# Optimization experiments

Hardware: AMD Instinct MI355X
Metric: run time of the kernel (lower is better)

## Reference

```python
import jax, jax.numpy as jnp
import numpy as np

B, C, L = 4, 512, 4096

def setup_inputs() -> dict:
    key = jax.random.key(0)
    k1, k2, k3, k4 = jax.random.split(key, 4)
    proj_query = jax.random.normal(k1, (B, C, L), dtype=jnp.float32)
    proj_key = jax.random.normal(k2, (B, C, L), dtype=jnp.float32)
    proj_val = jax.random.normal(k3, (B, C, L), dtype=jnp.float32)
    # binary padding mask over key positions, broadcast over query axis
    padding_mask = (jax.random.uniform(k4, (B, 1, L)) < 0.9).astype(jnp.float32)
    return {"proj_query": proj_query, "proj_key": proj_key,
            "proj_val": proj_val, "padding_mask": padding_mask}

def reference(proj_query, proj_key, proj_val, padding_mask):
    c = proj_query.shape[1]
    # energy[b,i,j] = sum_c Q[b,c,i] * K[b,c,j]  -> (B, L1, L2)
    energy = jnp.einsum('bci,bcj->bij', proj_query, proj_key)
    attention = energy / jnp.sqrt(jnp.asarray(c, dtype=energy.dtype))
    attention = attention + jnp.log(padding_mask + 1e-6)
    attention = jax.nn.softmax(attention, axis=-1)
    attention = attention * padding_mask
    attention = attention.transpose(0, 2, 1)  # (B, L2, L1)
    out = jnp.einsum('bcj,bji->bci', proj_val, attention)  # (B, C, L1)
    return out, attention
```

## Files before the change

kernel.cpp:

```cpp
#include <hip/hip_runtime.h>

#define B_ 4
#define C_ 512
#define L_ 4096

typedef __attribute__((ext_vector_type(8))) short bf16x8;
typedef __attribute__((ext_vector_type(4))) float f32x4;

static __device__ __forceinline__ unsigned short f2bf_rne(float f) {
  unsigned u = __float_as_uint(f);
  u += 0x7FFFu + ((u >> 16) & 1u);
  return (unsigned short)(u >> 16);
}
static __device__ __forceinline__ unsigned pack_rne(float a, float b) {
  return (unsigned)f2bf_rne(a) | ((unsigned)f2bf_rne(b) << 16);
}
static __device__ __forceinline__ unsigned pack_trunc(float a, float b) {
  return (__float_as_uint(a) >> 16) | (__float_as_uint(b) & 0xFFFF0000u);
}

static __device__ __forceinline__ void g2lds16(const unsigned short* g,
                                               unsigned short* l) {
  __builtin_amdgcn_global_load_lds(
      (const __attribute__((address_space(1))) unsigned int*)g,
      (__attribute__((address_space(3))) unsigned int*)l, 16, 0, 0);
}

__global__ __launch_bounds__(256) void transpose_cast_k(
    const float* __restrict__ Q, const float* __restrict__ K,
    unsigned short* __restrict__ Qt, unsigned short* __restrict__ Kt) {
  int zb = blockIdx.z;
  int b = zb >> 1;
  const float* src = ((zb & 1) ? K : Q) + (size_t)b * C_ * L_;
  unsigned short* dst = ((zb & 1) ? Kt : Qt) + (size_t)b * L_ * C_;
  int i0 = blockIdx.x * 64, c0 = blockIdx.y * 64;
  __shared__ float tile[64][65];
  int t = threadIdx.x;
  int cr = t >> 2, ig = (t & 3) * 16;
  const float* s = src + (size_t)(c0 + cr) * L_ + i0 + ig;
#pragma unroll
  for (int q = 0; q < 4; ++q) {
    float4 v = *(const float4*)(s + 4 * q);
    tile[cr][ig + 4 * q + 0] = v.x;
    tile[cr][ig + 4 * q + 1] = v.y;
    tile[cr][ig + 4 * q + 2] = v.z;
    tile[cr][ig + 4 * q + 3] = v.w;
  }
  __syncthreads();
  int ir = t >> 2, cg = (t & 3) * 16;
  unsigned wds[8];
#pragma unroll
  for (int k = 0; k < 8; ++k)
    wds[k] = pack_rne(tile[cg + 2 * k][ir], tile[cg + 2 * k + 1][ir]);
  unsigned short* d = dst + (size_t)(i0 + ir) * C_ + c0 + cg;
  uint4 o0, o1;
  o0.x = wds[0]; o0.y = wds[1]; o0.z = wds[2]; o0.w = wds[3];
  o1.x = wds[4]; o1.y = wds[5]; o1.z = wds[6]; o1.w = wds[7];
  *(uint4*)d = o0;
  *(uint4*)(d + 8) = o1;
}

__global__ __launch_bounds__(256) void cast_v_k(
    const float* __restrict__ V, const float* __restrict__ mask,
    unsigned short* __restrict__ Vb) {
  size_t idx = ((size_t)blockIdx.x * 256 + threadIdx.x) * 8;
  int b = (int)(idx >> 21);
  int j = (int)(idx & (L_ - 1));
  float4 v0 = *(const float4*)(V + idx);
  float4 v1 = *(const float4*)(V + idx + 4);
  const float* m = mask + (size_t)b * L_ + j;
  float4 m0 = *(const float4*)m;
  float4 m1 = *(const float4*)(m + 4);
  uint4 o;
  o.x = pack_rne(v0.x * m0.x, v0.y * m0.y);
  o.y = pack_rne(v0.z * m0.z, v0.w * m0.w);
  o.z = pack_rne(v1.x * m1.x, v1.y * m1.y);
  o.w = pack_rne(v1.z * m1.z, v1.w * m1.w);
  *(uint4*)(Vb + idx) = o;
}

__device__ __forceinline__ void gemm_mainloop(
    const unsigned short* Ab, const unsigned short* Bb, int lda, int ldb,
    int Kdim, unsigned short* sA, unsigned short* sB, f32x4 acc[4][4]) {
  int t = threadIdx.x;
  int f0 = t * 8;
  int f1 = 2048 + t * 8;
  int r0 = f0 >> 5, q0 = f0 & 31;
  int r1 = f1 >> 5, q1 = f1 & 31;
  const unsigned short* pA0 = Ab + (size_t)r0 * lda + q0;
  const unsigned short* pA1 = Ab + (size_t)r1 * lda + q1;
  const unsigned short* pB0 = Bb + (size_t)r0 * ldb + q0;
  const unsigned short* pB1 = Bb + (size_t)r1 * ldb + q1;
  int lane = t & 63;
  int quad = lane >> 4;
  int l15 = lane & 15;
  int w = t >> 6;
  int wm = (w & 1) * 64;
  int wn = (w >> 1) * 64;
  for (int kk = 0; kk < Kdim; kk += 32) {
    __syncthreads();
    g2lds16(pA0 + kk, sA + f0);
    g2lds16(pA1 + kk, sA + f1);
    g2lds16(pB0 + kk, sB + f0);
    g2lds16(pB1 + kk, sB + f1);
    __syncthreads();
    bf16x8 aF[4], bF[4];
#pragma unroll
    for (int ti = 0; ti < 4; ++ti)
      aF[ti] = *(const bf16x8*)(sA + (wm + ti * 16 + l15) * 32 + quad * 8);
#pragma unroll
    for (int tj = 0; tj < 4; ++tj)
      bF[tj] = *(const bf16x8*)(sB + (wn + tj * 16 + l15) * 32 + quad * 8);
#pragma unroll
    for (int ti = 0; ti < 4; ++ti)
#pragma unroll
      for (int tj = 0; tj < 4; ++tj)
        acc[ti][tj] = __builtin_amdgcn_mfma_f32_16x16x32_bf16(
            aF[ti], bF[tj], acc[ti][tj], 0, 0, 0);
  }
}

__global__ __launch_bounds__(256) void gemm1_k(
    const unsigned short* __restrict__ Qt, const unsigned short* __restrict__ Kt,
    const float* __restrict__ mask, float* __restrict__ attn,
    float* __restrict__ rowsum) {
  int b = blockIdx.z;
  int i0 = blockIdx.y * 128;
  int j0 = blockIdx.x * 128;
  __shared__ unsigned short sA[128 * 32];
  __shared__ unsigned short sB[128 * 32];
  f32x4 acc[4][4] = {};
  gemm_mainloop(Qt + (size_t)b * L_ * C_ + (size_t)i0 * C_,
                Kt + (size_t)b * L_ * C_ + (size_t)j0 * C_, C_, C_, C_, sA, sB,
                acc);
  int t = threadIdx.x;
  int lane = t & 63;
  int quad = lane >> 4;
  int l15 = lane & 15;
  int w = t >> 6;
  int wm = (w & 1) * 64;
  int wn = (w >> 1) * 64;
  const float scale = 0.04419417382415922f;
  float lm[4];
#pragma unroll
  for (int tj = 0; tj < 4; ++tj) {
    int j = j0 + wn + tj * 16 + l15;
    lm[tj] = __logf(mask[(size_t)b * L_ + j] + 1e-6f);
  }
  float* ab = attn + (size_t)b * L_ * L_;
  float rs[16];
#pragma unroll
  for (int q = 0; q < 16; ++q) rs[q] = 0.f;
#pragma unroll
  for (int ti = 0; ti < 4; ++ti) {
    int irow = i0 + wm + ti * 16 + quad * 4;
#pragma unroll
    for (int r = 0; r < 4; ++r) {
      size_t ro = (size_t)(irow + r) * L_;
#pragma unroll
      for (int tj = 0; tj < 4; ++tj) {
        float x = fminf(acc[ti][tj][r] * scale + lm[tj], 60.f);
        float tv = __expf(x);
        rs[ti * 4 + r] += tv;
        ab[ro + j0 + wn + tj * 16 + l15] = tv;
      }
    }
  }
#pragma unroll
  for (int m = 1; m < 16; m <<= 1)
#pragma unroll
    for (int q = 0; q < 16; ++q) rs[q] += __shfl_xor(rs[q], m, 64);
  if (l15 == 0) {
    float* rb = rowsum + (size_t)b * L_ + i0 + wm;
#pragma unroll
    for (int ti = 0; ti < 4; ++ti)
#pragma unroll
      for (int r = 0; r < 4; ++r)
        atomicAdd(&rb[ti * 16 + quad * 4 + r], rs[ti * 4 + r]);
  }
}

__global__ __launch_bounds__(256) void gemm2_k(
    const unsigned short* __restrict__ Vb, const float* __restrict__ tmat,
    const float* __restrict__ rowsum, float* __restrict__ out) {
  int b = blockIdx.z;
  int c0 = blockIdx.y * 128;
  int i0 = blockIdx.x * 128;
  __shared__ unsigned short sA[128 * 32];
  __shared__ unsigned short sB[128 * 32];
  const unsigned short* Ab = Vb + (size_t)b * C_ * L_ + (size_t)c0 * L_;
  const float* Bb = tmat + (size_t)b * L_ * L_ + (size_t)i0 * L_;
  int t = threadIdx.x;
  int f0 = t * 8;
  int f1 = 2048 + t * 8;
  int r0 = f0 >> 5, q0 = f0 & 31;
  int r1 = f1 >> 5, q1 = f1 & 31;
  const unsigned short* pA0 = Ab + (size_t)r0 * L_ + q0;
  const unsigned short* pA1 = Ab + (size_t)r1 * L_ + q1;
  const float* pB0 = Bb + (size_t)r0 * L_ + q0;
  const float* pB1 = Bb + (size_t)r1 * L_ + q1;
  int lane = t & 63;
  int quad = lane >> 4;
  int l15 = lane & 15;
  int w = t >> 6;
  int wm = (w & 1) * 64;
  int wn = (w >> 1) * 64;
  f32x4 acc[4][4] = {};
  for (int kk = 0; kk < L_; kk += 32) {
    __syncthreads();
    g2lds16(pA0 + kk, sA + f0);
    g2lds16(pA1 + kk, sA + f1);
    float4 x0 = *(const float4*)(pB0 + kk);
    float4 x1 = *(const float4*)(pB0 + kk + 4);
    float4 y0 = *(const float4*)(pB1 + kk);
    float4 y1 = *(const float4*)(pB1 + kk + 4);
    uint4 u0, u1;
    u0.x = pack_trunc(x0.x, x0.y); u0.y = pack_trunc(x0.z, x0.w);
    u0.z = pack_trunc(x1.x, x1.y); u0.w = pack_trunc(x1.z, x1.w);
    u1.x = pack_trunc(y0.x, y0.y); u1.y = pack_trunc(y0.z, y0.w);
    u1.z = pack_trunc(y1.x, y1.y); u1.w = pack_trunc(y1.z, y1.w);
    *(uint4*)(sB + f0) = u0;
    *(uint4*)(sB + f1) = u1;
    __syncthreads();
    bf16x8 aF[4], bF[4];
#pragma unroll
    for (int ti = 0; ti < 4; ++ti)
      aF[ti] = *(const bf16x8*)(sA + (wm + ti * 16 + l15) * 32 + quad * 8);
#pragma unroll
    for (int tj = 0; tj < 4; ++tj)
      bF[tj] = *(const bf16x8*)(sB + (wn + tj * 16 + l15) * 32 + quad * 8);
#pragma unroll
    for (int ti = 0; ti < 4; ++ti)
#pragma unroll
      for (int tj = 0; tj < 4; ++tj)
        acc[ti][tj] = __builtin_amdgcn_mfma_f32_16x16x32_bf16(
            aF[ti], bF[tj], acc[ti][tj], 0, 0, 0);
  }
  float invv[4];
#pragma unroll
  for (int tj = 0; tj < 4; ++tj)
    invv[tj] = 1.0f / rowsum[(size_t)b * L_ + i0 + wn + tj * 16 + l15];
  float* ob = out + (size_t)b * C_ * L_;
#pragma unroll
  for (int ti = 0; ti < 4; ++ti) {
    int crow = c0 + wm + ti * 16 + quad * 4;
#pragma unroll
    for (int r = 0; r < 4; ++r) {
      size_t ro = (size_t)(crow + r) * L_;
#pragma unroll
      for (int tj = 0; tj < 4; ++tj)
        ob[ro + i0 + wn + tj * 16 + l15] = acc[ti][tj][r] * invv[tj];
    }
  }
}

__global__ __launch_bounds__(256) void transpose_scale_k(
    float* __restrict__ attn, const float* __restrict__ rowsum,
    const float* __restrict__ mask) {
  int ti = blockIdx.x, tj = blockIdx.y;
  if (ti > tj) return;
  int b = blockIdx.z;
  float* M = attn + (size_t)b * L_ * L_;
  const float* mk = mask + (size_t)b * L_;
  const float* rs = rowsum + (size_t)b * L_;
  __shared__ float t1[64][65];
  __shared__ float t2[64][65];
  int t = threadIdx.x;
  int r = t >> 2, cg = (t & 3) * 16;
  bool diag = (ti == tj);
  {
    const float* xp = M + (size_t)(ti * 64 + r) * L_ + tj * 64 + cg;
    float invx = 1.0f / rs[ti * 64 + r];
    const float* mx = mk + tj * 64 + cg;
#pragma unroll
    for (int q = 0; q < 4; ++q) {
      float4 v = *(const float4*)(xp + 4 * q);
      float4 m = *(const float4*)(mx + 4 * q);
      t1[r][cg + 4 * q + 0] = v.x * m.x * invx;
      t1[r][cg + 4 * q + 1] = v.y * m.y * invx;
      t1[r][cg + 4 * q + 2] = v.z * m.z * invx;
      t1[r][cg + 4 * q + 3] = v.w * m.w * invx;
    }
  }
  if (!diag) {
    const float* yp = M + (size_t)(tj * 64 + r) * L_ + ti * 64 + cg;
    float invy = 1.0f / rs[tj * 64 + r];
    const float* my = mk + ti * 64 + cg;
#pragma unroll
    for (int q = 0; q < 4; ++q) {
      float4 v = *(const float4*)(yp + 4 * q);
      float4 m = *(const float4*)(my + 4 * q);
      t2[r][cg + 4 * q + 0] = v.x * m.x * invy;
      t2[r][cg + 4 * q + 1] = v.y * m.y * invy;
      t2[r][cg + 4 * q + 2] = v.z * m.z * invy;
      t2[r][cg + 4 * q + 3] = v.w * m.w * invy;
    }
  }
  __syncthreads();
  {
    float* dp = M + (size_t)(tj * 64 + r) * L_ + ti * 64 + cg;
#pragma unroll
    for (int q = 0; q < 4; ++q) {
      float4 o;
      o.x = t1[cg + 4 * q + 0][r];
      o.y = t1[cg + 4 * q + 1][r];
      o.z = t1[cg + 4 * q + 2][r];
      o.w = t1[cg + 4 * q + 3][r];
      *(float4*)(dp + 4 * q) = o;
    }
  }
  if (!diag) {
    float* dp = M + (size_t)(ti * 64 + r) * L_ + tj * 64 + cg;
#pragma unroll
    for (int q = 0; q < 4; ++q) {
      float4 o;
      o.x = t2[cg + 4 * q + 0][r];
      o.y = t2[cg + 4 * q + 1][r];
      o.z = t2[cg + 4 * q + 2][r];
      o.w = t2[cg + 4 * q + 3][r];
      *(float4*)(dp + 4 * q) = o;
    }
  }
}

extern "C" void kernel_launch(void* const* d_in, const int* in_sizes, int n_in,
                              void* d_out, int out_size, void* d_ws,
                              size_t ws_size, hipStream_t stream) {
  const float* Q = (const float*)d_in[0];
  const float* K = (const float*)d_in[1];
  const float* V = (const float*)d_in[2];
  const float* mask = (const float*)d_in[3];

  float* out = (float*)d_out;
  float* attn = out + (size_t)B_ * C_ * L_;

  unsigned short* Qt = (unsigned short*)d_ws;
  unsigned short* Kt = Qt + (size_t)B_ * L_ * C_;
  unsigned short* Vb = Kt + (size_t)B_ * L_ * C_;
  float* rowsum = (float*)(Vb + (size_t)B_ * C_ * L_);

  hipMemsetAsync(rowsum, 0, (size_t)B_ * L_ * sizeof(float), stream);

  transpose_cast_k<<<dim3(L_ / 64, C_ / 64, B_ * 2), 256, 0, stream>>>(Q, K, Qt,
                                                                       Kt);
  cast_v_k<<<dim3((B_ * C_ * L_) / 2048), 256, 0, stream>>>(V, mask, Vb);
  gemm1_k<<<dim3(L_ / 128, L_ / 128, B_), 256, 0, stream>>>(Qt, Kt, mask, attn,
                                                            rowsum);
  gemm2_k<<<dim3(L_ / 128, C_ / 128, B_), 256, 0, stream>>>(Vb, attn, rowsum,
                                                            out);
  transpose_scale_k<<<dim3(64, 64, B_), 256, 0, stream>>>(attn, rowsum, mask);
}
```

Baseline: 812.9 us.

## Store unnormalized attention as bf16 in scratch and split-K the PV GEMM

Gemm1 now writes exp-scores as bf16 into the upper halves of the attention output buffer and a workspace slot, in place of fp32 attention. This halves traffic for the intermediate matrix that gemm2 reads. Gemm2 is split into two K halves that accumulate into a zeroed output with atomics, doubling the grid. Per-batch finalize kernels then normalize and transpose the bf16 data into fp32 attention. The gains come with an extra memset, atomic traffic on the output, a dependence on the workspace size, and ordering hazards from aliasing inside the output buffer.

```diff
diff --git a/kernel.cpp b/kernel.cpp
--- a/kernel.cpp
+++ b/kernel.cpp
@@ -17,6 +17,12 @@
 }
 static __device__ __forceinline__ unsigned pack_trunc(float a, float b) {
   return (__float_as_uint(a) >> 16) | (__float_as_uint(b) & 0xFFFF0000u);
+}
+static __device__ __forceinline__ float bflo2f(unsigned w) {
+  return __uint_as_float(w << 16);
+}
+static __device__ __forceinline__ float bfhi2f(unsigned w) {
+  return __uint_as_float(w & 0xFFFF0000u);
 }
 
 static __device__ __forceinline__ void g2lds16(const unsigned short* g,
@@ -117,6 +123,148 @@
       for (int tj = 0; tj < 4; ++tj)
         acc[ti][tj] = __builtin_amdgcn_mfma_f32_16x16x32_bf16(
             aF[ti], bF[tj], acc[ti][tj], 0, 0, 0);
+  }
+}
+
+
+__global__ __launch_bounds__(256) void gemm1_bf_k(
+    const unsigned short* __restrict__ Qt, const unsigned short* __restrict__ Kt,
+    const float* __restrict__ mask, unsigned short* __restrict__ t0,
+    unsigned short* __restrict__ t1, unsigned short* __restrict__ t2,
+    unsigned short* __restrict__ t3, float* __restrict__ rowsum) {
+  int b = blockIdx.z;
+  unsigned short* tbb = (b == 0) ? t0 : (b == 1) ? t1 : (b == 2) ? t2 : t3;
+  int i0 = blockIdx.y * 128;
+  int j0 = blockIdx.x * 128;
+  __shared__ unsigned short sA[128 * 32];
+  __shared__ unsigned short sB[128 * 32];
+  f32x4 acc[4][4] = {};
+  gemm_mainloop(Qt + (size_t)b * L_ * C_ + (size_t)i0 * C_,
+                Kt + (size_t)b * L_ * C_ + (size_t)j0 * C_, C_, C_, C_, sA, sB,
+                acc);
+  int t = threadIdx.x;
+  int lane = t & 63;
+  int quad = lane >> 4;
+  int l15 = lane & 15;
+  int w = t >> 6;
+  int wm = (w & 1) * 64;
+  int wn = (w >> 1) * 64;
+  const float scale = 0.04419417382415922f;
+  float lm[4], mv[4];
+#pragma unroll
+  for (int tj = 0; tj < 4; ++tj) {
+    int j = j0 + wn + tj * 16 + l15;
+    float m = mask[(size_t)b * L_ + j];
+    mv[tj] = m;
+    lm[tj] = __logf(m + 1e-6f);
+  }
+  float rs[16];
+#pragma unroll
+  for (int q = 0; q < 16; ++q) rs[q] = 0.f;
+#pragma unroll
+  for (int ti = 0; ti < 4; ++ti) {
+    int irow = i0 + wm + ti * 16 + quad * 4;
+#pragma unroll
+    for (int r = 0; r < 4; ++r) {
+      size_t ro = (size_t)(irow + r) * L_;
+#pragma unroll
+      for (int tj = 0; tj < 4; ++tj) {
+        float x = fminf(acc[ti][tj][r] * scale + lm[tj], 60.f);
+        float tv = __expf(x);
+        rs[ti * 4 + r] += tv;
+        tbb[ro + j0 + wn + tj * 16 + l15] = f2bf_rne(tv * mv[tj]);
+      }
+    }
+  }
+#pragma unroll
+  for (int m = 1; m < 16; m <<= 1)
+#pragma unroll
+    for (int q = 0; q < 16; ++q) rs[q] += __shfl_xor(rs[q], m, 64);
+  if (l15 == 0) {
+    float* rb = rowsum + (size_t)b * L_ + i0 + wm;
+#pragma unroll
+    for (int ti = 0; ti < 4; ++ti)
+#pragma unroll
+      for (int r = 0; r < 4; ++r)
+        atomicAdd(&rb[ti * 16 + quad * 4 + r], rs[ti * 4 + r]);
+  }
+}
+
+__global__ __launch_bounds__(256) void gemm2_bf_k(
+    const unsigned short* __restrict__ Vb, const unsigned short* __restrict__ t0,
+    const unsigned short* __restrict__ t1, const unsigned short* __restrict__ t2,
+    const unsigned short* __restrict__ t3, const float* __restrict__ rowsum,
+    float* __restrict__ out) {
+  int z = blockIdx.z;
+  int b = z & 3;
+  int ks = z >> 2;
+  const unsigned short* tbb =
+      (b == 0) ? t0 : (b == 1) ? t1 : (b == 2) ? t2 : t3;
+  int c0 = blockIdx.y * 128;
+  int i0 = blockIdx.x * 128;
+  __shared__ unsigned short sA[128 * 32];
+  __shared__ unsigned short sB[128 * 32];
+  f32x4 acc[4][4] = {};
+  gemm_mainloop(Vb + (size_t)b * C_ * L_ + (size_t)c0 * L_ + ks * (L_ / 2),
+                tbb + (size_t)i0 * L_ + ks * (L_ / 2), L_, L_, L_ / 2, sA, sB,
+                acc);
+  int t = threadIdx.x;
+  int lane = t & 63;
+  int quad = lane >> 4;
+  int l15 = lane & 15;
+  int w = t >> 6;
+  int wm = (w & 1) * 64;
+  int wn = (w >> 1) * 64;
+  float invv[4];
+#pragma unroll
+  for (int tj = 0; tj < 4; ++tj)
+    invv[tj] = 1.0f / rowsum[(size_t)b * L_ + i0 + wn + tj * 16 + l15];
+  float* ob = out + (size_t)b * C_ * L_;
+#pragma unroll
+  for (int ti = 0; ti < 4; ++ti) {
+    int crow = c0 + wm + ti * 16 + quad * 4;
+#pragma unroll
+    for (int r = 0; r < 4; ++r) {
+      size_t ro = (size_t)(crow + r) * L_;
+#pragma unroll
+      for (int tj = 0; tj < 4; ++tj)
+        atomicAdd(&ob[ro + i0 + wn + tj * 16 + l15],
+                  acc[ti][tj][r] * invv[tj]);
+    }
+  }
+}
+
+__global__ __launch_bounds__(256) void finalize_k(
+    const unsigned short* __restrict__ src, const float* __restrict__ rs,
+    float* __restrict__ dst) {
+  int jt = blockIdx.x, it = blockIdx.y;
+  __shared__ float tileT[64][65];
+  int t = threadIdx.x;
+  int r = t >> 2, cg = (t & 3) * 16;
+  int i = it * 64 + r;
+  float inv = 1.0f / rs[i];
+  const unsigned short* sp = src + (size_t)i * L_ + jt * 64 + cg;
+  uint4 u0 = *(const uint4*)sp;
+  uint4 u1 = *(const uint4*)(sp + 8);
+  const unsigned* w0 = (const unsigned*)&u0;
+  const unsigned* w1 = (const unsigned*)&u1;
+#pragma unroll
+  for (int k = 0; k < 4; ++k) {
+    tileT[cg + 2 * k + 0][r] = bflo2f(w0[k]) * inv;
+    tileT[cg + 2 * k + 1][r] = bfhi2f(w0[k]) * inv;
+    tileT[cg + 8 + 2 * k + 0][r] = bflo2f(w1[k]) * inv;
+    tileT[cg + 8 + 2 * k + 1][r] = bfhi2f(w1[k]) * inv;
+  }
+  __syncthreads();
+  float* dp = dst + (size_t)(jt * 64 + r) * L_ + it * 64 + cg;
+#pragma unroll
+  for (int q = 0; q < 4; ++q) {
+    float4 o;
+    o.x = tileT[r][cg + 4 * q + 0];
+    o.y = tileT[r][cg + 4 * q + 1];
+    o.z = tileT[r][cg + 4 * q + 2];
+    o.w = tileT[r][cg + 4 * q + 3];
+    *(float4*)(dp + 4 * q) = o;
   }
 }
 
@@ -334,19 +482,43 @@
   float* out = (float*)d_out;
   float* attn = out + (size_t)B_ * C_ * L_;
 
+  const size_t NQ = (size_t)B_ * L_ * C_;
   unsigned short* Qt = (unsigned short*)d_ws;
-  unsigned short* Kt = Qt + (size_t)B_ * L_ * C_;
-  unsigned short* Vb = Kt + (size_t)B_ * L_ * C_;
-  float* rowsum = (float*)(Vb + (size_t)B_ * C_ * L_);
+  unsigned short* Kt = Qt + NQ;
+  unsigned short* Vb = Kt + NQ;
+  float* rowsum = (float*)(Vb + NQ);
+  unsigned short* tb3 = (unsigned short*)(rowsum + (size_t)B_ * L_);
+
+  const size_t need = NQ * 2 * 3 + (size_t)B_ * L_ * 4 + (size_t)L_ * L_ * 2;
 
   hipMemsetAsync(rowsum, 0, (size_t)B_ * L_ * sizeof(float), stream);
-
   transpose_cast_k<<<dim3(L_ / 64, C_ / 64, B_ * 2), 256, 0, stream>>>(Q, K, Qt,
                                                                        Kt);
   cast_v_k<<<dim3((B_ * C_ * L_) / 2048), 256, 0, stream>>>(V, mask, Vb);
-  gemm1_k<<<dim3(L_ / 128, L_ / 128, B_), 256, 0, stream>>>(Qt, Kt, mask, attn,
-                                                            rowsum);
-  gemm2_k<<<dim3(L_ / 128, C_ / 128, B_), 256, 0, stream>>>(Vb, attn, rowsum,
-                                                            out);
-  transpose_scale_k<<<dim3(64, 64, B_), 256, 0, stream>>>(attn, rowsum, mask);
-}
+
+  if (ws_size >= need) {
+    const size_t SLOT = (size_t)L_ * L_;
+    unsigned short* tb0 = (unsigned short*)(attn + 2 * SLOT);
+    unsigned short* tb1 = (unsigned short*)(attn + 3 * SLOT);
+    unsigned short* tb2 = (unsigned short*)(attn + 3 * SLOT + SLOT / 2);
+    hipMemsetAsync(out, 0, (size_t)B_ * C_ * L_ * sizeof(float), stream);
+    gemm1_bf_k<<<dim3(L_ / 128, L_ / 128, B_), 256, 0, stream>>>(
+        Qt, Kt, mask, tb0, tb1, tb2, tb3, rowsum);
+    gemm2_bf_k<<<dim3(L_ / 128, C_ / 128, B_ * 2), 256, 0, stream>>>(
+        Vb, tb0, tb1, tb2, tb3, rowsum, out);
+    finalize_k<<<dim3(64, 64), 256, 0, stream>>>(tb0, rowsum, attn);
+    finalize_k<<<dim3(64, 64), 256, 0, stream>>>(tb1, rowsum + L_,
+                                                 attn + 1 * SLOT);
+    finalize_k<<<dim3(64, 64), 256, 0, stream>>>(tb2, rowsum + 2 * L_,
+                                                 attn + 2 * SLOT);
+    finalize_k<<<dim3(64, 64), 256, 0, stream>>>(tb3, rowsum + 3 * L_,
+                                                 attn + 3 * SLOT);
+  } else {
+    gemm1_k<<<dim3(L_ / 128, L_ / 128, B_), 256, 0, stream>>>(Qt, Kt, mask,
+                                                              attn, rowsum);
+    gemm2_k<<<dim3(L_ / 128, C_ / 128, B_), 256, 0, stream>>>(Vb, attn, rowsum,
+                                                              out);
+    transpose_scale_k<<<dim3(64, 64, B_), 256, 0, stream>>>(attn, rowsum,
+                                                            mask);
+  }
+}
```

Measured after the change: 719.8 us. -11.5%, faster.

## Store unnormalized masked attention as bf16 and split-K gemm2 with tiled transpose finalize

Applied to the files above, without the earlier changes.

GEMM1 now writes the masked exponentials as bf16 into a workspace instead of fp32 into the output, which halves that intermediate's traffic. GEMM2 reads the bf16 tiles directly through global_load_lds instead of loading fp32 and packing in registers, and splits K in two across the grid with a combine pass. The shared mainloop now stages 64-wide K chunks per barrier pair, and a new finalize kernel normalizes and transposes the bf16 into the fp32 attention output over the full grid. A fallback path aliases buffers into the output and uses atomics when the workspace is too small; rounding the probabilities to bf16 before the fp32 attention output adds rounding error.

```diff
diff --git a/kernel.cpp b/kernel.cpp
--- a/kernel.cpp
+++ b/kernel.cpp
@@ -15,8 +15,11 @@
 static __device__ __forceinline__ unsigned pack_rne(float a, float b) {
   return (unsigned)f2bf_rne(a) | ((unsigned)f2bf_rne(b) << 16);
 }
-static __device__ __forceinline__ unsigned pack_trunc(float a, float b) {
-  return (__float_as_uint(a) >> 16) | (__float_as_uint(b) & 0xFFFF0000u);
+static __device__ __forceinline__ float bflo2f(unsigned w) {
+  return __uint_as_float(w << 16);
+}
+static __device__ __forceinline__ float bfhi2f(unsigned w) {
+  return __uint_as_float(w & 0xFFFF0000u);
 }
 
 static __device__ __forceinline__ void g2lds16(const unsigned short* g,
@@ -79,60 +82,72 @@
   *(uint4*)(Vb + idx) = o;
 }
 
-__device__ __forceinline__ void gemm_mainloop(
+__device__ __forceinline__ void gemm_mainloop64(
     const unsigned short* Ab, const unsigned short* Bb, int lda, int ldb,
     int Kdim, unsigned short* sA, unsigned short* sB, f32x4 acc[4][4]) {
   int t = threadIdx.x;
-  int f0 = t * 8;
-  int f1 = 2048 + t * 8;
-  int r0 = f0 >> 5, q0 = f0 & 31;
-  int r1 = f1 >> 5, q1 = f1 & 31;
-  const unsigned short* pA0 = Ab + (size_t)r0 * lda + q0;
-  const unsigned short* pA1 = Ab + (size_t)r1 * lda + q1;
-  const unsigned short* pB0 = Bb + (size_t)r0 * ldb + q0;
-  const unsigned short* pB1 = Bb + (size_t)r1 * ldb + q1;
+  const unsigned short* pA[4];
+  const unsigned short* pB[4];
+#pragma unroll
+  for (int c = 0; c < 4; ++c) {
+    int e = t * 8 + c * 2048;
+    int kc = e >> 12;
+    int rem = e & 4095;
+    int row = rem >> 5;
+    int col = rem & 31;
+    int off = kc * 32 + col;
+    pA[c] = Ab + (size_t)row * lda + off;
+    pB[c] = Bb + (size_t)row * ldb + off;
+  }
   int lane = t & 63;
   int quad = lane >> 4;
   int l15 = lane & 15;
   int w = t >> 6;
   int wm = (w & 1) * 64;
   int wn = (w >> 1) * 64;
-  for (int kk = 0; kk < Kdim; kk += 32) {
+  for (int kk = 0; kk < Kdim; kk += 64) {
     __syncthreads();
-    g2lds16(pA0 + kk, sA + f0);
-    g2lds16(pA1 + kk, sA + f1);
-    g2lds16(pB0 + kk, sB + f0);
-    g2lds16(pB1 + kk, sB + f1);
+#pragma unroll
+    for (int c = 0; c < 4; ++c) g2lds16(pA[c] + kk, sA + t * 8 + c * 2048);
+#pragma unroll
+    for (int c = 0; c < 4; ++c) g2lds16(pB[c] + kk, sB + t * 8 + c * 2048);
     __syncthreads();
-    bf16x8 aF[4], bF[4];
-#pragma unroll
-    for (int ti = 0; ti < 4; ++ti)
-      aF[ti] = *(const bf16x8*)(sA + (wm + ti * 16 + l15) * 32 + quad * 8);
-#pragma unroll
-    for (int tj = 0; tj < 4; ++tj)
-      bF[tj] = *(const bf16x8*)(sB + (wn + tj * 16 + l15) * 32 + quad * 8);
-#pragma unroll
-    for (int ti = 0; ti < 4; ++ti)
+#pragma unroll
+    for (int kc = 0; kc < 2; ++kc) {
+      bf16x8 aF[4], bF[4];
+#pragma unroll
+      for (int ti = 0; ti < 4; ++ti)
+        aF[ti] = *(const bf16x8*)(sA + kc * 4096 +
+                                  (wm + ti * 16 + l15) * 32 + quad * 8);
 #pragma unroll
       for (int tj = 0; tj < 4; ++tj)
-        acc[ti][tj] = __builtin_amdgcn_mfma_f32_16x16x32_bf16(
-            aF[ti], bF[tj], acc[ti][tj], 0, 0, 0);
-  }
-}
-
-__global__ __launch_bounds__(256) void gemm1_k(
+        bF[tj] = *(const bf16x8*)(sB + kc * 4096 +
+                                  (wn + tj * 16 + l15) * 32 + quad * 8);
+#pragma unroll
+      for (int ti = 0; ti < 4; ++ti)
+#pragma unroll
+        for (int tj = 0; tj < 4; ++tj)
+          acc[ti][tj] = __builtin_amdgcn_mfma_f32_16x16x32_bf16(
+              aF[ti], bF[tj], acc[ti][tj], 0, 0, 0);
+    }
+  }
+}
+
+__global__ __launch_bounds__(256) void gemm1_bf_k(
     const unsigned short* __restrict__ Qt, const unsigned short* __restrict__ Kt,
-    const float* __restrict__ mask, float* __restrict__ attn,
-    float* __restrict__ rowsum) {
+    const float* __restrict__ mask, unsigned short* __restrict__ t0,
+    unsigned short* __restrict__ t1, unsigned short* __restrict__ t2,
+    unsigned short* __restrict__ t3, float* __restrict__ rowsum) {
   int b = blockIdx.z;
+  unsigned short* tbb = (b == 0) ? t0 : (b == 1) ? t1 : (b == 2) ? t2 : t3;
   int i0 = blockIdx.y * 128;
   int j0 = blockIdx.x * 128;
-  __shared__ unsigned short sA[128 * 32];
-  __shared__ unsigned short sB[128 * 32];
+  __shared__ unsigned short sA[8192];
+  __shared__ unsigned short sB[8192];
   f32x4 acc[4][4] = {};
-  gemm_mainloop(Qt + (size_t)b * L_ * C_ + (size_t)i0 * C_,
-                Kt + (size_t)b * L_ * C_ + (size_t)j0 * C_, C_, C_, C_, sA, sB,
-                acc);
+  gemm_mainloop64(Qt + (size_t)b * L_ * C_ + (size_t)i0 * C_,
+                  Kt + (size_t)b * L_ * C_ + (size_t)j0 * C_, C_, C_, C_, sA,
+                  sB, acc);
   int t = threadIdx.x;
   int lane = t & 63;
   int quad = lane >> 4;
@@ -141,13 +156,14 @@
   int wm = (w & 1) * 64;
   int wn = (w >> 1) * 64;
   const float scale = 0.04419417382415922f;
-  float lm[4];
+  float lm[4], mv[4];
 #pragma unroll
   for (int tj = 0; tj < 4; ++tj) {
     int j = j0 + wn + tj * 16 + l15;
-    lm[tj] = __logf(mask[(size_t)b * L_ + j] + 1e-6f);
-  }
-  float* ab = attn + (size_t)b * L_ * L_;
+    float m = mask[(size_t)b * L_ + j];
+    mv[tj] = m;
+    lm[tj] = __logf(m + 1e-6f);
+  }
   float rs[16];
 #pragma unroll
   for (int q = 0; q < 16; ++q) rs[q] = 0.f;
@@ -162,7 +178,7 @@
         float x = fminf(acc[ti][tj][r] * scale + lm[tj], 60.f);
         float tv = __expf(x);
         rs[ti * 4 + r] += tv;
-        ab[ro + j0 + wn + tj * 16 + l15] = tv;
+        tbb[ro + j0 + wn + tj * 16 + l15] = f2bf_rne(tv * mv[tj]);
       }
     }
   }
@@ -180,67 +196,37 @@
   }
 }
 
-__global__ __launch_bounds__(256) void gemm2_k(
-    const unsigned short* __restrict__ Vb, const float* __restrict__ tmat,
-    const float* __restrict__ rowsum, float* __restrict__ out) {
-  int b = blockIdx.z;
+template <bool ATOMIC>
+__global__ __launch_bounds__(256) void gemm2_bf_k(
+    const unsigned short* __restrict__ Vb, const unsigned short* __restrict__ t0,
+    const unsigned short* __restrict__ t1, const unsigned short* __restrict__ t2,
+    const unsigned short* __restrict__ t3, const float* __restrict__ rowsum,
+    float* __restrict__ out, float* __restrict__ out2) {
+  int z = blockIdx.z;
+  int b = z & 3;
+  int ks = z >> 2;
+  const unsigned short* tbb =
+      (b == 0) ? t0 : (b == 1) ? t1 : (b == 2) ? t2 : t3;
   int c0 = blockIdx.y * 128;
   int i0 = blockIdx.x * 128;
-  __shared__ unsigned short sA[128 * 32];
-  __shared__ unsigned short sB[128 * 32];
-  const unsigned short* Ab = Vb + (size_t)b * C_ * L_ + (size_t)c0 * L_;
-  const float* Bb = tmat + (size_t)b * L_ * L_ + (size_t)i0 * L_;
-  int t = threadIdx.x;
-  int f0 = t * 8;
-  int f1 = 2048 + t * 8;
-  int r0 = f0 >> 5, q0 = f0 & 31;
-  int r1 = f1 >> 5, q1 = f1 & 31;
-  const unsigned short* pA0 = Ab + (size_t)r0 * L_ + q0;
-  const unsigned short* pA1 = Ab + (size_t)r1 * L_ + q1;
-  const float* pB0 = Bb + (size_t)r0 * L_ + q0;
-  const float* pB1 = Bb + (size_t)r1 * L_ + q1;
+  __shared__ unsigned short sA[8192];
+  __shared__ unsigned short sB[8192];
+  f32x4 acc[4][4] = {};
+  gemm_mainloop64(Vb + (size_t)b * C_ * L_ + (size_t)c0 * L_ + ks * (L_ / 2),
+                  tbb + (size_t)i0 * L_ + ks * (L_ / 2), L_, L_, L_ / 2, sA, sB,
+                  acc);
+  int t = threadIdx.x;
   int lane = t & 63;
   int quad = lane >> 4;
   int l15 = lane & 15;
   int w = t >> 6;
   int wm = (w & 1) * 64;
   int wn = (w >> 1) * 64;
-  f32x4 acc[4][4] = {};
-  for (int kk = 0; kk < L_; kk += 32) {
-    __syncthreads();
-    g2lds16(pA0 + kk, sA + f0);
-    g2lds16(pA1 + kk, sA + f1);
-    float4 x0 = *(const float4*)(pB0 + kk);
-    float4 x1 = *(const float4*)(pB0 + kk + 4);
-    float4 y0 = *(const float4*)(pB1 + kk);
-    float4 y1 = *(const float4*)(pB1 + kk + 4);
-    uint4 u0, u1;
-    u0.x = pack_trunc(x0.x, x0.y); u0.y = pack_trunc(x0.z, x0.w);
-    u0.z = pack_trunc(x1.x, x1.y); u0.w = pack_trunc(x1.z, x1.w);
-    u1.x = pack_trunc(y0.x, y0.y); u1.y = pack_trunc(y0.z, y0.w);
-    u1.z = pack_trunc(y1.x, y1.y); u1.w = pack_trunc(y1.z, y1.w);
-    *(uint4*)(sB + f0) = u0;
-    *(uint4*)(sB + f1) = u1;
-    __syncthreads();
-    bf16x8 aF[4], bF[4];
-#pragma unroll
-    for (int ti = 0; ti < 4; ++ti)
-      aF[ti] = *(const bf16x8*)(sA + (wm + ti * 16 + l15) * 32 + quad * 8);
-#pragma unroll
-    for (int tj = 0; tj < 4; ++tj)
-      bF[tj] = *(const bf16x8*)(sB + (wn + tj * 16 + l15) * 32 + quad * 8);
-#pragma unroll
-    for (int ti = 0; ti < 4; ++ti)
-#pragma unroll
-      for (int tj = 0; tj < 4; ++tj)
-        acc[ti][tj] = __builtin_amdgcn_mfma_f32_16x16x32_bf16(
-            aF[ti], bF[tj], acc[ti][tj], 0, 0, 0);
-  }
   float invv[4];
 #pragma unroll
   for (int tj = 0; tj < 4; ++tj)
     invv[tj] = 1.0f / rowsum[(size_t)b * L_ + i0 + wn + tj * 16 + l15];
-  float* ob = out + (size_t)b * C_ * L_;
+  float* ob = (ATOMIC ? out : (ks ? out2 : out)) + (size_t)b * C_ * L_;
 #pragma unroll
   for (int ti = 0; ti < 4; ++ti) {
     int crow = c0 + wm + ti * 16 + quad * 4;
@@ -248,78 +234,65 @@
     for (int r = 0; r < 4; ++r) {
       size_t ro = (size_t)(crow + r) * L_;
 #pragma unroll
-      for (int tj = 0; tj < 4; ++tj)
-        ob[ro + i0 + wn + tj * 16 + l15] = acc[ti][tj][r] * invv[tj];
+      for (int tj = 0; tj < 4; ++tj) {
+        float v = acc[ti][tj][r] * invv[tj];
+        if (ATOMIC)
+          atomicAdd(&ob[ro + i0 + wn + tj * 16 + l15], v);
+        else
+          ob[ro + i0 + wn + tj * 16 + l15] = v;
+      }
     }
   }
 }
 
-__global__ __launch_bounds__(256) void transpose_scale_k(
-    float* __restrict__ attn, const float* __restrict__ rowsum,
-    const float* __restrict__ mask) {
-  int ti = blockIdx.x, tj = blockIdx.y;
-  if (ti > tj) return;
+__global__ __launch_bounds__(256) void combine_out_k(
+    float* __restrict__ out, const float* __restrict__ out2) {
+  size_t idx = ((size_t)blockIdx.x * 256 + threadIdx.x) * 8;
+  float4 a0 = *(const float4*)(out + idx);
+  float4 a1 = *(const float4*)(out + idx + 4);
+  float4 b0 = *(const float4*)(out2 + idx);
+  float4 b1 = *(const float4*)(out2 + idx + 4);
+  a0.x += b0.x; a0.y += b0.y; a0.z += b0.z; a0.w += b0.w;
+  a1.x += b1.x; a1.y += b1.y; a1.z += b1.z; a1.w += b1.w;
+  *(float4*)(out + idx) = a0;
+  *(float4*)(out + idx + 4) = a1;
+}
+
+__global__ __launch_bounds__(256) void finalize_all_k(
+    const unsigned short* __restrict__ tb, const float* __restrict__ rowsum,
+    float* __restrict__ attn) {
   int b = blockIdx.z;
-  float* M = attn + (size_t)b * L_ * L_;
-  const float* mk = mask + (size_t)b * L_;
+  const unsigned short* src = tb + (size_t)b * L_ * L_;
   const float* rs = rowsum + (size_t)b * L_;
-  __shared__ float t1[64][65];
-  __shared__ float t2[64][65];
+  float* dst = attn + (size_t)b * L_ * L_;
+  int jt = blockIdx.x, it = blockIdx.y;
+  __shared__ float tileT[64][65];
   int t = threadIdx.x;
   int r = t >> 2, cg = (t & 3) * 16;
-  bool diag = (ti == tj);
-  {
-    const float* xp = M + (size_t)(ti * 64 + r) * L_ + tj * 64 + cg;
-    float invx = 1.0f / rs[ti * 64 + r];
-    const float* mx = mk + tj * 64 + cg;
-#pragma unroll
-    for (int q = 0; q < 4; ++q) {
-      float4 v = *(const float4*)(xp + 4 * q);
-      float4 m = *(const float4*)(mx + 4 * q);
-      t1[r][cg + 4 * q + 0] = v.x * m.x * invx;
-      t1[r][cg + 4 * q + 1] = v.y * m.y * invx;
-      t1[r][cg + 4 * q + 2] = v.z * m.z * invx;
-      t1[r][cg + 4 * q + 3] = v.w * m.w * invx;
-    }
-  }
-  if (!diag) {
-    const float* yp = M + (size_t)(tj * 64 + r) * L_ + ti * 64 + cg;
-    float invy = 1.0f / rs[tj * 64 + r];
-    const float* my = mk + ti * 64 + cg;
-#pragma unroll
-    for (int q = 0; q < 4; ++q) {
-      float4 v = *(const float4*)(yp + 4 * q);
-      float4 m = *(const float4*)(my + 4 * q);
-      t2[r][cg + 4 * q + 0] = v.x * m.x * invy;
-      t2[r][cg + 4 * q + 1] = v.y * m.y * invy;
-      t2[r][cg + 4 * q + 2] = v.z * m.z * invy;
-      t2[r][cg + 4 * q + 3] = v.w * m.w * invy;
-    }
+  int i = it * 64 + r;
+  float inv = 1.0f / rs[i];
+  const unsigned short* sp = src + (size_t)i * L_ + jt * 64 + cg;
+  uint4 u0 = *(const uint4*)sp;
+  uint4 u1 = *(const uint4*)(sp + 8);
+  const unsigned* w0 = (const unsigned*)&u0;
+  const unsigned* w1 = (const unsigned*)&u1;
+#pragma unroll
+  for (int k = 0; k < 4; ++k) {
+    tileT[cg + 2 * k + 0][r] = bflo2f(w0[k]) * inv;
+    tileT[cg + 2 * k + 1][r] = bfhi2f(w0[k]) * inv;
+    tileT[cg + 8 + 2 * k + 0][r] = bflo2f(w1[k]) * inv;
+    tileT[cg + 8 + 2 * k + 1][r] = bfhi2f(w1[k]) * inv;
   }
   __syncthreads();
-  {
-    float* dp = M + (size_t)(tj * 64 + r) * L_ + ti * 64 + cg;
-#pragma unroll
-    for (int q = 0; q < 4; ++q) {
-      float4 o;
-      o.x = t1[cg + 4 * q + 0][r];
-      o.y = t1[cg + 4 * q + 1][r];
-      o.z = t1[cg + 4 * q + 2][r];
-      o.w = t1[cg + 4 * q + 3][r];
-      *(float4*)(dp + 4 * q) = o;
-    }
-  }
-  if (!diag) {
-    float* dp = M + (size_t)(ti * 64 + r) * L_ + tj * 64 + cg;
-#pragma unroll
-    for (int q = 0; q < 4; ++q) {
-      float4 o;
-      o.x = t2[cg + 4 * q + 0][r];
-      o.y = t2[cg + 4 * q + 1][r];
-      o.z = t2[cg + 4 * q + 2][r];
-      o.w = t2[cg + 4 * q + 3][r];
-      *(float4*)(dp + 4 * q) = o;
-    }
+  float* dp = dst + (size_t)(jt * 64 + r) * L_ + it * 64 + cg;
+#pragma unroll
+  for (int q = 0; q < 4; ++q) {
+    float4 o;
+    o.x = tileT[r][cg + 4 * q + 0];
+    o.y = tileT[r][cg + 4 * q + 1];
+    o.z = tileT[r][cg + 4 * q + 2];
+    o.w = tileT[r][cg + 4 * q + 3];
+    *(float4*)(dp + 4 * q) = o;
   }
 }
 
@@ -334,19 +307,47 @@
   float* out = (float*)d_out;
   float* attn = out + (size_t)B_ * C_ * L_;
 
+  const size_t NQ = (size_t)B_ * L_ * C_;
+  const size_t SLOT = (size_t)L_ * L_;
   unsigned short* Qt = (unsigned short*)d_ws;
-  unsigned short* Kt = Qt + (size_t)B_ * L_ * C_;
-  unsigned short* Vb = Kt + (size_t)B_ * L_ * C_;
-  float* rowsum = (float*)(Vb + (size_t)B_ * C_ * L_);
+  unsigned short* Kt = Qt + NQ;
+  unsigned short* Vb = Kt + NQ;
+  float* rowsum = (float*)(Vb + NQ);
+  unsigned short* wtail = (unsigned short*)(rowsum + (size_t)B_ * L_);
+
+  const size_t need1 =
+      NQ * 2 * 3 + (size_t)B_ * L_ * 4 + (size_t)B_ * SLOT * 2 + NQ * 4;
 
   hipMemsetAsync(rowsum, 0, (size_t)B_ * L_ * sizeof(float), stream);
-
   transpose_cast_k<<<dim3(L_ / 64, C_ / 64, B_ * 2), 256, 0, stream>>>(Q, K, Qt,
                                                                        Kt);
   cast_v_k<<<dim3((B_ * C_ * L_) / 2048), 256, 0, stream>>>(V, mask, Vb);
-  gemm1_k<<<dim3(L_ / 128, L_ / 128, B_), 256, 0, stream>>>(Qt, Kt, mask, attn,
-                                                            rowsum);
-  gemm2_k<<<dim3(L_ / 128, C_ / 128, B_), 256, 0, stream>>>(Vb, attn, rowsum,
-                                                            out);
-  transpose_scale_k<<<dim3(64, 64, B_), 256, 0, stream>>>(attn, rowsum, mask);
-}
+
+  if (ws_size >= need1) {
+    unsigned short* tb = wtail;
+    float* out2 = (float*)(tb + (size_t)B_ * SLOT);
+    gemm1_bf_k<<<dim3(L_ / 128, L_ / 128, B_), 256, 0, stream>>>(
+        Qt, Kt, mask, tb, tb + SLOT, tb + 2 * SLOT, tb + 3 * SLOT, rowsum);
+    gemm2_bf_k<false><<<dim3(L_ / 128, C_ / 128, B_ * 2), 256, 0, stream>>>(
+        Vb, tb, tb + SLOT, tb + 2 * SLOT, tb + 3 * SLOT, rowsum, out, out2);
+    combine_out_k<<<dim3((B_ * C_ * L_) / 2048), 256, 0, stream>>>(out, out2);
+    finalize_all_k<<<dim3(64, 64, B_), 256, 0, stream>>>(tb, rowsum, attn);
+  } else {
+    unsigned short* tb0 = (unsigned short*)(attn + 2 * SLOT);
+    unsigned short* tb1 = (unsigned short*)(attn + 3 * SLOT);
+    unsigned short* tb2 = (unsigned short*)(attn + 3 * SLOT + SLOT / 2);
+    unsigned short* tb3 = wtail;
+    hipMemsetAsync(out, 0, (size_t)B_ * C_ * L_ * sizeof(float), stream);
+    gemm1_bf_k<<<dim3(L_ / 128, L_ / 128, B_), 256, 0, stream>>>(
+        Qt, Kt, mask, tb0, tb1, tb2, tb3, rowsum);
+    gemm2_bf_k<true><<<dim3(L_ / 128, C_ / 128, B_ * 2), 256, 0, stream>>>(
+        Vb, tb0, tb1, tb2, tb3, rowsum, out, out);
+    finalize_all_k<<<dim3(64, 64, 1), 256, 0, stream>>>(tb0, rowsum, attn);
+    finalize_all_k<<<dim3(64, 64, 1), 256, 0, stream>>>(tb1, rowsum + L_,
+                                                        attn + SLOT);
+    finalize_all_k<<<dim3(64, 64, 1), 256, 0, stream>>>(tb2, rowsum + 2 * L_,
+                                                        attn + 2 * SLOT);
+    finalize_all_k<<<dim3(64, 64, 1), 256, 0, stream>>>(tb3, rowsum + 3 * L_,
+                                                        attn + 3 * SLOT);
+  }
+}
```

Result: faster. 668.7 us (-17.7%).
